# Performance work log

Hardware: AMD Instinct MI355X
Metric: run time of the kernel (lower is better)

## Reference

```python
import math
import jax, jax.numpy as jnp
import numpy as np

B, T, C = 2, 2048, 1024
H, Ca = 16, 64


def setup_inputs() -> dict:
    key = jax.random.key(0)
    ks = jax.random.split(key, 5)
    # kaiming-uniform-ish scale for weights
    wb = 1.0 / math.sqrt(C)
    return {
        "x": jax.random.normal(ks[0], (B, T, C), dtype=jnp.float32),
        "w_q": jax.random.uniform(ks[1], (H, C, Ca), jnp.float32, -wb, wb),
        "w_k": jax.random.uniform(ks[2], (H, C, Ca), jnp.float32, -wb, wb),
        "w_v": jax.random.uniform(ks[3], (H, C, Ca), jnp.float32, -wb, wb),
        "w_o": jax.random.uniform(ks[4], (C, C), jnp.float32, -wb, wb),
    }


def reference(x, w_q, w_k, w_v, w_o):
    # x: [B,T,C]; w_q/w_k/w_v: [H,C,Ca]; w_o: [C,C]
    scale = 1.0 / math.sqrt(w_q.shape[-1])
    q = jnp.einsum("btc,hca->bhta", x, w_q)  # [B,H,T,Ca]
    k = jnp.einsum("btc,hca->bhta", x, w_k)
    v = jnp.einsum("btc,hca->bhta", x, w_v)
    s = jnp.einsum("bhta,bhsa->bhts", q, k)  # [B,H,T,T]
    # faithful to original: mask where tril(s)==0, scale applied after masking
    s_hat = jnp.where(jnp.tril(s) == 0, -jnp.inf, s * scale)
    a = jax.nn.softmax(s_hat, axis=-1)
    y = jnp.einsum("bhts,bhsa->bhta", a, v)  # [B,H,T,Ca]
    y_cat = y.transpose(0, 2, 1, 3).reshape(x.shape)  # [B,T,C]
    return y_cat @ w_o
```

## Files before the change

kernel.cpp:

```cpp
#include <hip/hip_runtime.h>
#include <stdint.h>

#define Bc 2
#define Tc 2048
#define Cn 1024
#define Hc 16
#define CAc 64

typedef __attribute__((ext_vector_type(8))) short short8;
typedef __attribute__((ext_vector_type(4))) float f32x4;

__device__ __forceinline__ unsigned short f2bf(float f) {
    unsigned int u = __builtin_bit_cast(unsigned int, f);
    return (unsigned short)((u + 0x7fffu + ((u >> 16) & 1u)) >> 16);
}

__device__ __forceinline__ void async_cp16(const unsigned short* g, unsigned short* l) {
    __builtin_amdgcn_global_load_lds(
        (const __attribute__((address_space(1))) unsigned int*)g,
        (__attribute__((address_space(3))) unsigned int*)l,
        16, 0, 0);
}

__global__ __launch_bounds__(256) void detect_dtype(
    const unsigned short* __restrict__ x, int* __restrict__ flag)
{
    __shared__ int cnt;
    if (threadIdx.x == 0) cnt = 0;
    __syncthreads();
    int c = 0;
#pragma unroll
    for (int i = 0; i < 8; i++) {
        int idx = (threadIdx.x * 8 + i) * 2;
        unsigned short u = x[idx];
        int e = (u >> 7) & 0xFF;
        if (e >= 0x68 && e <= 0x90) c++;
    }
    atomicAdd(&cnt, c);
    __syncthreads();
    if (threadIdx.x == 0) *flag = (cnt > 1024) ? 1 : 0;
}

__global__ __launch_bounds__(256) void convert_x(
    const void* __restrict__ xin, unsigned short* __restrict__ xb,
    const int* __restrict__ flag)
{
    int idx = (blockIdx.x * 256 + threadIdx.x) * 4;
    if (*flag) {
        *(uint2*)(&xb[idx]) = *(const uint2*)((const unsigned short*)xin + idx);
    } else {
        const float* xf = (const float*)xin;
        float4 v = *(const float4*)(xf + idx);
        union { unsigned short s[4]; uint2 u; } p;
        p.s[0] = f2bf(v.x); p.s[1] = f2bf(v.y); p.s[2] = f2bf(v.z); p.s[3] = f2bf(v.w);
        *(uint2*)(&xb[idx]) = p.u;
    }
}

__device__ __forceinline__ unsigned short ld_elem(const void* base, size_t off, int isbf) {
    return isbf ? ((const unsigned short*)base)[off] : f2bf(((const float*)base)[off]);
}

__global__ __launch_bounds__(256) void transpose_weights(
    const void* __restrict__ wq, const void* __restrict__ wk,
    const void* __restrict__ wv, const void* __restrict__ wo,
    unsigned short* __restrict__ wT, unsigned short* __restrict__ woT,
    const int* __restrict__ flag)
{
    const int isbf = *flag;
    __shared__ unsigned short tile[32][33];
    const int bx = blockIdx.x;
    const int t = threadIdx.x;
    const int tx = t & 31, ty = t >> 5;
    const void* src;
    unsigned short* dst;
    int R, Cw, r0, c0;
    if (bx < 3072) {
        int g = bx >> 6;
        int rem = bx & 63;
        int ct = rem >> 1;
        int at = rem & 1;
        int proj = g >> 4, h = g & 15;
        const void* wsel = (proj == 0) ? wq : ((proj == 1) ? wk : wv);
        src = isbf ? (const void*)((const unsigned short*)wsel + (size_t)h * Cn * CAc)
                   : (const void*)((const float*)wsel + (size_t)h * Cn * CAc);
        dst = wT + (size_t)g * CAc * Cn;
        R = Cn; Cw = CAc; r0 = ct * 32; c0 = at * 32;
    } else {
        int rem = bx - 3072;
        src = wo; dst = woT;
        R = Cn; Cw = Cn;
        r0 = (rem >> 5) * 32; c0 = (rem & 31) * 32;
    }
#pragma unroll
    for (int j = 0; j < 4; j++)
        tile[ty + j * 8][tx] = ld_elem(src, (size_t)(r0 + ty + j * 8) * Cw + c0 + tx, isbf);
    __syncthreads();
#pragma unroll
    for (int j = 0; j < 4; j++)
        dst[(size_t)(c0 + ty + j * 8) * R + r0 + tx] = tile[tx][ty + j * 8];
}

template <int MODE>
__global__ __launch_bounds__(256) void gemm128(
    const unsigned short* __restrict__ Amat,
    const unsigned short* __restrict__ Bt,
    void* __restrict__ o0,
    unsigned short* __restrict__ o1,
    unsigned short* __restrict__ o2,
    const int* __restrict__ flag)
{
    const int LDA = 40;
    __shared__ alignas(16) unsigned short Al[128 * LDA];
    __shared__ alignas(16) unsigned short Bl[128 * LDA];
    const int tid = threadIdx.x;
    const int wave = tid >> 6, lane = tid & 63;
    const int l15 = lane & 15, quad = lane >> 4;
    const int mBase = blockIdx.y * 128, nBase = blockIdx.x * 128;
    const int mOff = (wave & 1) * 64, nOff = (wave >> 1) * 64;

    f32x4 acc[4][4];
#pragma unroll
    for (int i = 0; i < 4; i++)
#pragma unroll
        for (int j = 0; j < 4; j++)
            acc[i][j] = (f32x4){0.f, 0.f, 0.f, 0.f};

    for (int k0 = 0; k0 < Cn; k0 += 32) {
#pragma unroll
        for (int c = 0; c < 2; c++) {
            int idx = c * 256 + tid;
            int row = idx >> 2, col = (idx & 3) * 8;
            *(uint4*)(&Al[row * LDA + col]) =
                *(const uint4*)(&Amat[(size_t)(mBase + row) * Cn + k0 + col]);
            *(uint4*)(&Bl[row * LDA + col]) =
                *(const uint4*)(&Bt[(size_t)(nBase + row) * Cn + k0 + col]);
        }
        __syncthreads();
        short8 af[4], bfr[4];
#pragma unroll
        for (int i = 0; i < 4; i++)
            af[i] = *(const short8*)(&Al[(mOff + i * 16 + l15) * LDA + quad * 8]);
#pragma unroll
        for (int j = 0; j < 4; j++)
            bfr[j] = *(const short8*)(&Bl[(nOff + j * 16 + l15) * LDA + quad * 8]);
#pragma unroll
        for (int i = 0; i < 4; i++)
#pragma unroll
            for (int j = 0; j < 4; j++)
                acc[i][j] = __builtin_amdgcn_mfma_f32_16x16x32_bf16(af[i], bfr[j], acc[i][j], 0, 0, 0);
        __syncthreads();
    }

    if constexpr (MODE == 0) {
#pragma unroll
        for (int i = 0; i < 4; i++) {
            int m0 = mBase + mOff + i * 16 + quad * 4;
            int b = m0 >> 11, t0 = m0 & (Tc - 1);
#pragma unroll
            for (int j = 0; j < 4; j++) {
                int n = nBase + nOff + j * 16 + l15;
                int proj = n >> 10, h = (n >> 6) & 15, a = n & 63;
                if (proj == 2) {
                    union { unsigned short s[4]; uint2 v; } pk;
#pragma unroll
                    for (int r = 0; r < 4; r++) pk.s[r] = f2bf(acc[i][j][r]);
                    *(uint2*)(&o2[((size_t)(b * Hc + h) * CAc + a) * Tc + t0]) = pk.v;
                } else {
                    unsigned short* dst = (proj == 0) ? (unsigned short*)o0 : o1;
                    size_t base = ((size_t)(b * Hc + h) * Tc + t0) * CAc + a;
#pragma unroll
                    for (int r = 0; r < 4; r++)
                        dst[base + (size_t)r * CAc] = f2bf(acc[i][j][r]);
                }
            }
        }
    } else {
        const int isbf = *flag;
#pragma unroll
        for (int i = 0; i < 4; i++) {
            int m0 = mBase + mOff + i * 16 + quad * 4;
#pragma unroll
            for (int j = 0; j < 4; j++) {
                int n = nBase + nOff + j * 16 + l15;
                if (isbf) {
#pragma unroll
                    for (int r = 0; r < 4; r++)
                        ((unsigned short*)o0)[(size_t)(m0 + r) * Cn + n] = f2bf(acc[i][j][r]);
                } else {
#pragma unroll
                    for (int r = 0; r < 4; r++)
                        ((float*)o0)[(size_t)(m0 + r) * Cn + n] = acc[i][j][r];
                }
            }
        }
    }
}

__global__ __launch_bounds__(256) void attn_pair(
    const unsigned short* __restrict__ q,
    const unsigned short* __restrict__ k,
    const unsigned short* __restrict__ vT,
    unsigned short* __restrict__ y)
{
    __shared__ alignas(16) unsigned short Kl[2][64 * 64];
    __shared__ alignas(16) unsigned short Vl[2][64 * 64];
    const int LDP = 72;
    __shared__ alignas(16) unsigned short Pl[4][16 * LDP];
    const int bx = blockIdx.x;
    const int pr = bx & 15, bh = bx >> 4;
    const int h = bh & 15, b = bh >> 4;
    const int qt1 = pr, qt2 = 31 - pr;
    const int tid = threadIdx.x;
    const int wave = tid >> 6, lane = tid & 63;
    const int l15 = lane & 15, quad = lane >> 4;
    const int m0w1 = qt1 * 64 + wave * 16;
    const int m0w2 = qt2 * 64 + wave * 16;
    const size_t bhoff = (size_t)(b * Hc + h);
    const unsigned short* qh = q + bhoff * Tc * CAc;
    const unsigned short* kh = k + bhoff * Tc * CAc;
    const unsigned short* vh = vT + bhoff * CAc * Tc;

    const int srow = (lane >> 3);
    const int sgc  = (lane & 7) ^ srow;
    const int h7 = l15 & 7;
    const int sw0 = ((quad ^ h7) << 3);
    const int sw1 = (((4 + quad) ^ h7) << 3);

    short8 qf1[2], qf2[2];
#pragma unroll
    for (int s = 0; s < 2; s++) {
        qf1[s] = *(const short8*)(&qh[(size_t)(m0w1 + l15) * CAc + s * 32 + quad * 8]);
        qf2[s] = *(const short8*)(&qh[(size_t)(m0w2 + l15) * CAc + s * 32 + quad * 8]);
    }

    f32x4 oacc1[4], oacc2[4], osum1, osum2;
#pragma unroll
    for (int j2 = 0; j2 < 4; j2++) {
        oacc1[j2] = (f32x4){0.f, 0.f, 0.f, 0.f};
        oacc2[j2] = (f32x4){0.f, 0.f, 0.f, 0.f};
    }
    osum1 = (f32x4){0.f, 0.f, 0.f, 0.f};
    osum2 = (f32x4){0.f, 0.f, 0.f, 0.f};

    const unsigned short ONE = 0x3F80;
    short8 ones;
#pragma unroll
    for (int i = 0; i < 8; i++) ones[i] = (short)ONE;

    unsigned short* Pw = &Pl[wave][0];

#pragma unroll
    for (int t = 0; t < 2; t++) {
        int rl = wave * 16 + t * 8;
        async_cp16(kh + (size_t)(rl + srow) * CAc + sgc * 8, &Kl[0][rl * 64]);
        async_cp16(vh + (size_t)(rl + srow) * Tc  + sgc * 8, &Vl[0][rl * 64]);
    }
    __syncthreads();

    for (int kt = 0; kt <= qt2; kt++) {
        const int k0 = kt * 64;
        const int cur = kt & 1;
        const bool act1 = (kt <= qt1);
        if (kt < qt2) {
            const unsigned short* kg = kh + (size_t)(k0 + 64) * CAc;
            const unsigned short* vg = vh + (k0 + 64);
#pragma unroll
            for (int t = 0; t < 2; t++) {
                int rl = wave * 16 + t * 8;
                async_cp16(kg + (size_t)(rl + srow) * CAc + sgc * 8, &Kl[1 - cur][rl * 64]);
                async_cp16(vg + (size_t)(rl + srow) * Tc  + sgc * 8, &Vl[1 - cur][rl * 64]);
            }
        }
        const unsigned short* Kc = Kl[cur];
        const unsigned short* Vc = Vl[cur];

        float s1[4][4], s2[4][4];
#pragma unroll
        for (int j = 0; j < 4; j++) {
            short8 kf0 = *(const short8*)(&Kc[(j * 16 + l15) * 64 + sw0]);
            short8 kf1 = *(const short8*)(&Kc[(j * 16 + l15) * 64 + sw1]);
            f32x4 z2 = (f32x4){0.f, 0.f, 0.f, 0.f};
            z2 = __builtin_amdgcn_mfma_f32_16x16x32_bf16(kf0, qf2[0], z2, 0, 0, 0);
            z2 = __builtin_amdgcn_mfma_f32_16x16x32_bf16(kf1, qf2[1], z2, 0, 0, 0);
#pragma unroll
            for (int r = 0; r < 4; r++) s2[j][r] = z2[r];
            if (act1) {
                f32x4 z1 = (f32x4){0.f, 0.f, 0.f, 0.f};
                z1 = __builtin_amdgcn_mfma_f32_16x16x32_bf16(kf0, qf1[0], z1, 0, 0, 0);
                z1 = __builtin_amdgcn_mfma_f32_16x16x32_bf16(kf1, qf1[1], z1, 0, 0, 0);
#pragma unroll
                for (int r = 0; r < 4; r++) s1[j][r] = z1[r];
            }
        }

        if (kt == qt2) {
            int tg = m0w2 + l15;
#pragma unroll
            for (int j = 0; j < 4; j++)
#pragma unroll
                for (int r = 0; r < 4; r++) {
                    int sg = k0 + j * 16 + quad * 4 + r;
                    s2[j][r] = (sg <= tg) ? __expf(fminf(s2[j][r] * 0.125f, 80.f)) : 0.f;
                }
        } else {
#pragma unroll
            for (int j = 0; j < 4; j++)
#pragma unroll
                for (int r = 0; r < 4; r++)
                    s2[j][r] = __expf(fminf(s2[j][r] * 0.125f, 80.f));
        }
        if (act1) {
            if (kt == qt1) {
                int tg = m0w1 + l15;
#pragma unroll
                for (int j = 0; j < 4; j++)
#pragma unroll
                    for (int r = 0; r < 4; r++) {
                        int sg = k0 + j * 16 + quad * 4 + r;
                        s1[j][r] = (sg <= tg) ? __expf(fminf(s1[j][r] * 0.125f, 80.f)) : 0.f;
                    }
            } else {
#pragma unroll
                for (int j = 0; j < 4; j++)
#pragma unroll
                    for (int r = 0; r < 4; r++)
                        s1[j][r] = __expf(fminf(s1[j][r] * 0.125f, 80.f));
            }
        }

        short8 pa2[2], pa1[2];
#pragma unroll
        for (int j = 0; j < 4; j++) {
            union { unsigned int d[2]; uint2 v; } pk;
            pk.d[0] = (unsigned int)f2bf(s2[j][0]) | ((unsigned int)f2bf(s2[j][1]) << 16);
            pk.d[1] = (unsigned int)f2bf(s2[j][2]) | ((unsigned int)f2bf(s2[j][3]) << 16);
            *(uint2*)(&Pw[l15 * LDP + j * 16 + quad * 4]) = pk.v;
        }
#pragma unroll
        for (int c = 0; c < 2; c++)
            pa2[c] = *(const short8*)(&Pw[l15 * LDP + c * 32 + quad * 8]);
        if (act1) {
#pragma unroll
            for (int j = 0; j < 4; j++) {
                union { unsigned int d[2]; uint2 v; } pk;
                pk.d[0] = (unsigned int)f2bf(s1[j][0]) | ((unsigned int)f2bf(s1[j][1]) << 16);
                pk.d[1] = (unsigned int)f2bf(s1[j][2]) | ((unsigned int)f2bf(s1[j][3]) << 16);
                *(uint2*)(&Pw[l15 * LDP + j * 16 + quad * 4]) = pk.v;
            }
#pragma unroll
            for (int c = 0; c < 2; c++)
                pa1[c] = *(const short8*)(&Pw[l15 * LDP + c * 32 + quad * 8]);
        }

#pragma unroll
        for (int c = 0; c < 2; c++) {
#pragma unroll
            for (int j2 = 0; j2 < 4; j2++) {
                short8 vb = *(const short8*)(&Vc[(j2 * 16 + l15) * 64 + (c ? sw1 : sw0)]);
                oacc2[j2] = __builtin_amdgcn_mfma_f32_16x16x32_bf16(pa2[c], vb, oacc2[j2], 0, 0, 0);
                if (act1)
                    oacc1[j2] = __builtin_amdgcn_mfma_f32_16x16x32_bf16(pa1[c], vb, oacc1[j2], 0, 0, 0);
            }
            osum2 = __builtin_amdgcn_mfma_f32_16x16x32_bf16(pa2[c], ones, osum2, 0, 0, 0);
            if (act1)
                osum1 = __builtin_amdgcn_mfma_f32_16x16x32_bf16(pa1[c], ones, osum1, 0, 0, 0);
        }
        __syncthreads();
    }

    float ri1[4], ri2[4];
#pragma unroll
    for (int r = 0; r < 4; r++) { ri1[r] = 1.0f / osum1[r]; ri2[r] = 1.0f / osum2[r]; }
#pragma unroll
    for (int j2 = 0; j2 < 4; j2++) {
#pragma unroll
        for (int r = 0; r < 4; r++) {
            int t1 = m0w1 + quad * 4 + r;
            int t2 = m0w2 + quad * 4 + r;
            y[((size_t)b * Tc + t1) * Cn + h * CAc + j2 * 16 + l15] = f2bf(oacc1[j2][r] * ri1[r]);
            y[((size_t)b * Tc + t2) * Cn + h * CAc + j2 * 16 + l15] = f2bf(oacc2[j2][r] * ri2[r]);
        }
    }
}

extern "C" void kernel_launch(void* const* d_in, const int* in_sizes, int n_in,
                              void* d_out, int out_size, void* d_ws, size_t ws_size,
                              hipStream_t stream) {
    const void* x  = d_in[0];
    const void* wq = d_in[1];
    const void* wk = d_in[2];
    const void* wv = d_in[3];
    const void* wo = d_in[4];
    char* ws = (char*)d_ws;
    int* flag = (int*)(ws);
    unsigned short* wT  = (unsigned short*)(ws + ((size_t)1 << 20));
    unsigned short* woT = (unsigned short*)(ws + ((size_t)7 << 20));
    unsigned short* xb  = (unsigned short*)(ws + ((size_t)9 << 20));
    unsigned short* qb  = (unsigned short*)(ws + ((size_t)17 << 20));
    unsigned short* kb  = (unsigned short*)(ws + ((size_t)25 << 20));
    unsigned short* vTb = (unsigned short*)(ws + ((size_t)33 << 20));
    unsigned short* yb  = (unsigned short*)(ws + ((size_t)41 << 20));

    detect_dtype<<<dim3(1), dim3(256), 0, stream>>>((const unsigned short*)x, flag);
    convert_x<<<dim3(4096), dim3(256), 0, stream>>>(x, xb, flag);
    transpose_weights<<<dim3(4096), dim3(256), 0, stream>>>(wq, wk, wv, wo, wT, woT, flag);
    gemm128<0><<<dim3(24, 32), dim3(256), 0, stream>>>(xb, wT, qb, kb, vTb, flag);
    attn_pair<<<dim3(512), dim3(256), 0, stream>>>(qb, kb, vTb, yb);
    gemm128<1><<<dim3(8, 32), dim3(256), 0, stream>>>(yb, woT, d_out, nullptr, nullptr, flag);
}
```

Before: 212.2 us.

## Double-buffer GEMM tiles with async global-to-LDS loads and XOR swizzle

Replaces the synchronous register-staged tile loads in the 128x128 GEMM with global_load_lds async copies into double-buffered LDS. The next K-slice is prefetched while the current one is consumed, and a padding-free XOR swizzle is meant to avoid LDS bank conflicts. Separately, the fminf clamp before exp in the attention softmax is dropped, saving a few ALU ops but risking overflow if scores grow large. The diff does not show the end-of-loop synchronization, so whether the buffer swap is correctly fenced depends on unseen code.

```diff
diff --git a/kernel.cpp b/kernel.cpp
--- a/kernel.cpp
+++ b/kernel.cpp
@@ -110,15 +110,18 @@
     unsigned short* __restrict__ o2,
     const int* __restrict__ flag)
 {
-    const int LDA = 40;
-    __shared__ alignas(16) unsigned short Al[128 * LDA];
-    __shared__ alignas(16) unsigned short Bl[128 * LDA];
+    __shared__ alignas(16) unsigned short Al[2][128 * 32];
+    __shared__ alignas(16) unsigned short Bl[2][128 * 32];
     const int tid = threadIdx.x;
     const int wave = tid >> 6, lane = tid & 63;
     const int l15 = lane & 15, quad = lane >> 4;
     const int mBase = blockIdx.y * 128, nBase = blockIdx.x * 128;
     const int mOff = (wave & 1) * 64, nOff = (wave >> 1) * 64;
 
+    const int srow = lane >> 2;
+    const int sgc  = (lane & 3) ^ (srow & 3);
+    const int sw = (quad ^ (l15 & 3)) * 8;
+
     f32x4 acc[4][4];
 #pragma unroll
     for (int i = 0; i < 4; i++)
@@ -126,24 +129,32 @@
         for (int j = 0; j < 4; j++)
             acc[i][j] = (f32x4){0.f, 0.f, 0.f, 0.f};
 
-    for (int k0 = 0; k0 < Cn; k0 += 32) {
-#pragma unroll
-        for (int c = 0; c < 2; c++) {
-            int idx = c * 256 + tid;
-            int row = idx >> 2, col = (idx & 3) * 8;
-            *(uint4*)(&Al[row * LDA + col]) =
-                *(const uint4*)(&Amat[(size_t)(mBase + row) * Cn + k0 + col]);
-            *(uint4*)(&Bl[row * LDA + col]) =
-                *(const uint4*)(&Bt[(size_t)(nBase + row) * Cn + k0 + col]);
-        }
-        __syncthreads();
+#pragma unroll
+    for (int t = 0; t < 2; t++) {
+        int rl = wave * 32 + t * 16;
+        async_cp16(Amat + (size_t)(mBase + rl + srow) * Cn + sgc * 8, &Al[0][rl * 32]);
+        async_cp16(Bt   + (size_t)(nBase + rl + srow) * Cn + sgc * 8, &Bl[0][rl * 32]);
+    }
+    __syncthreads();
+
+    for (int kk = 0; kk < 32; kk++) {
+        const int cur = kk & 1;
+        if (kk < 31) {
+            const int k1 = (kk + 1) * 32;
+#pragma unroll
+            for (int t = 0; t < 2; t++) {
+                int rl = wave * 32 + t * 16;
+                async_cp16(Amat + (size_t)(mBase + rl + srow) * Cn + k1 + sgc * 8, &Al[1 - cur][rl * 32]);
+                async_cp16(Bt   + (size_t)(nBase + rl + srow) * Cn + k1 + sgc * 8, &Bl[1 - cur][rl * 32]);
+            }
+        }
         short8 af[4], bfr[4];
 #pragma unroll
         for (int i = 0; i < 4; i++)
-            af[i] = *(const short8*)(&Al[(mOff + i * 16 + l15) * LDA + quad * 8]);
+            af[i] = *(const short8*)(&Al[cur][(mOff + i * 16 + l15) * 32 + sw]);
 #pragma unroll
         for (int j = 0; j < 4; j++)
-            bfr[j] = *(const short8*)(&Bl[(nOff + j * 16 + l15) * LDA + quad * 8]);
+            bfr[j] = *(const short8*)(&Bl[cur][(nOff + j * 16 + l15) * 32 + sw]);
 #pragma unroll
         for (int i = 0; i < 4; i++)
 #pragma unroll
@@ -301,14 +312,14 @@
 #pragma unroll
                 for (int r = 0; r < 4; r++) {
                     int sg = k0 + j * 16 + quad * 4 + r;
-                    s2[j][r] = (sg <= tg) ? __expf(fminf(s2[j][r] * 0.125f, 80.f)) : 0.f;
+                    s2[j][r] = (sg <= tg) ? __expf(s2[j][r] * 0.125f) : 0.f;
                 }
         } else {
 #pragma unroll
             for (int j = 0; j < 4; j++)
 #pragma unroll
                 for (int r = 0; r < 4; r++)
-                    s2[j][r] = __expf(fminf(s2[j][r] * 0.125f, 80.f));
+                    s2[j][r] = __expf(s2[j][r] * 0.125f);
         }
         if (act1) {
             if (kt == qt1) {
@@ -318,14 +329,14 @@
 #pragma unroll
                     for (int r = 0; r < 4; r++) {
                         int sg = k0 + j * 16 + quad * 4 + r;
-                        s1[j][r] = (sg <= tg) ? __expf(fminf(s1[j][r] * 0.125f, 80.f)) : 0.f;
+                        s1[j][r] = (sg <= tg) ? __expf(s1[j][r] * 0.125f) : 0.f;
                     }
             } else {
 #pragma unroll
                 for (int j = 0; j < 4; j++)
 #pragma unroll
                     for (int r = 0; r < 4; r++)
-                        s1[j][r] = __expf(fminf(s1[j][r] * 0.125f, 80.f));
+                        s1[j][r] = __expf(s1[j][r] * 0.125f);
             }
         }
 
```

Result: no change. 211.8 us (-0.2%).
